# Optimization experiments

Measured on AMD Instinct MI355X. Metric: run time of the kernel, lower is better.

## Reference

```python
import jax, jax.numpy as jnp
import numpy as np


def setup_inputs() -> dict:
    key = jax.random.key(0)
    k1, k2, k3 = jax.random.split(key, 3)
    n_way, n_shot, d, n_query = 5, 10, 1024, 16384
    n_support = n_way * n_shot
    train_imgs = jax.random.normal(k1, (n_support, d), dtype=jnp.float32)
    # one-hot labels: exactly n_shot examples per class (interleaved)
    cls = jnp.tile(jnp.arange(n_way), n_shot)  # [n_support]
    train_labels = jax.nn.one_hot(cls, n_way, dtype=jnp.int64)
    query_imgs = jax.random.normal(k2, (n_query, d), dtype=jnp.float32)
    query_labels = jax.random.randint(k3, (n_query,), 0, n_way)
    return {"train_imgs": train_imgs, "train_labels": train_labels,
            "query_imgs": query_imgs, "query_labels": query_labels}


def reference(train_imgs, train_labels, query_imgs, query_labels):
    # backbone = identity: imgs are already feature embeddings
    n_support, n_way = train_labels.shape
    n_shot = n_support // n_way  # static
    support = train_imgs                      # [n_support, d]
    query = query_imgs                        # [n_query, d]

    # group support features by class: [n_way, n_shot, d]
    cls = jnp.argmax(train_labels, axis=1)
    order = jnp.argsort(cls, stable=True)
    grouped = support[order].reshape(n_way, n_shot, -1)
    mats = jnp.swapaxes(grouped, 1, 2)        # [n_way, d, n_shot]

    # batched reduced SVD (torch.svd some=True -> full_matrices=False)
    U, _, _ = jnp.linalg.svd(mats, full_matrices=False)  # [n_way, d, n_shot]
    Uk = U[:, :, : n_shot - 1]                # [n_way, d, k]

    # projection of queries onto each class subspace: P = Uk Uk^T q
    coeff = jnp.einsum('wdk,qd->wkq', Uk, query)   # [n_way, k, n_query]
    proj = jnp.einsum('wdk,wkq->wqd', Uk, coeff)   # [n_way, n_query, d]
    dist = jnp.sum((query[None, :, :] - proj) ** 2, axis=-1)  # [n_way, n_query]

    logits = -dist.T                           # [n_query, n_way]
    # normalize=False in this configuration
    return jax.nn.log_softmax(logits, axis=1)
```

## Files before the change

kernel.cpp:

```cpp
#include <hip/hip_runtime.h>
#include <stdint.h>


typedef __attribute__((ext_vector_type(4))) float f32x4;
typedef __attribute__((ext_vector_type(8))) short s16x8;

#define WS_G_OFF    0
#define WS_W_OFF    4096
#define WS_IDX_OFF  6400
#define WS_U_OFF    8192

__device__ __forceinline__ unsigned short f2bf(float f) {
  unsigned int u = __float_as_uint(f);
  u += 0x7FFFu + ((u >> 16) & 1u);
  return (unsigned short)(u >> 16);
}

__device__ __forceinline__ bool labels_int64(const int* L) {
  int cnt = 0; bool oddz = true;
  #pragma unroll
  for (int t = 0; t < 20; ++t) {
    int v = L[t];
    if (t & 1) { if (v) oddz = false; }
    else       { if (v) cnt++; }
  }
  return oddz && (cnt == 2);
}

__device__ __forceinline__ int cls_of(const int* L, bool is64, int i) {
  int best = -0x7fffffff, c = 0;
  #pragma unroll
  for (int j = 0; j < 5; ++j) {
    int v = is64 ? L[i * 10 + 2 * j] : L[i * 5 + j];
    if (v > best) { best = v; c = j; }
  }
  return c;
}

__global__ void dsn_gram(const float* __restrict__ support,
                         const int* __restrict__ labels,
                         double* __restrict__ G,
                         int* __restrict__ idx) {
  int wid  = blockIdx.x * 4 + (threadIdx.x >> 6);
  int lane = threadIdx.x & 63;
  if (wid >= 275) return;
  int w = wid / 55, p = wid % 55;
  int a = 0;
  while (p >= 10 - a) { p -= 10 - a; a++; }
  int b = a + p;

  bool is64 = labels_int64(labels);
  int myc = (lane < 50) ? cls_of(labels, is64, lane) : -1;
  unsigned long long mask = __ballot(lane < 50 && myc == w);

  if (wid % 55 == 0 && lane < 10) {
    unsigned long long m2 = mask;
    for (int z = 0; z < lane; ++z) m2 &= m2 - 1;
    idx[w * 10 + lane] = __ffsll(m2) - 1;
  }

  unsigned long long m = mask;
  for (int i = 0; i < a; ++i) m &= m - 1;
  int ia = __ffsll((unsigned long long)m) - 1;
  m = mask;
  for (int i = 0; i < b; ++i) m &= m - 1;
  int ib = __ffsll((unsigned long long)m) - 1;

  const float* A = support + ia * 1024;
  const float* B = support + ib * 1024;
  double acc = 0.0;
  #pragma unroll
  for (int i = 0; i < 16; ++i) {
    int d = lane + 64 * i;
    acc += (double)A[d] * (double)B[d];
  }
  #pragma unroll
  for (int off = 32; off > 0; off >>= 1) acc += __shfl_xor(acc, off);
  if (lane == 0) {
    G[(w * 10 + a) * 10 + b] = acc;
    G[(w * 10 + b) * 10 + a] = acc;
  }
}

__global__ __launch_bounds__(64, 1) void dsn_solve(const double* __restrict__ G,
                                                   float* __restrict__ W) {
  __shared__ float Gf[100], Ysm[100], Zsm[100], Psm[100];
  __shared__ float red[16];
  __shared__ int   jm[1];

  int w = blockIdx.x, t = threadIdx.x;
  bool act = (t < 50);
  int e0 = 2 * t, e1 = 2 * t + 1;
  int i0 = e0 / 10, j0 = e0 % 10;
  int i1 = e1 / 10, j1 = e1 % 10;
  if (!act) { e0 = 0; e1 = 1; i0 = 0; j0 = 0; i1 = 0; j1 = 1; }

  if (act) {
    Gf[e0] = (float)G[w * 100 + e0];
    Gf[e1] = (float)G[w * 100 + e1];
  }
  __syncthreads();

  if (t < 10) {
    float r = 0.f;
    #pragma unroll
    for (int k = 0; k < 10; ++k) r += fabsf(Gf[t * 10 + k]);
    red[t] = r;
  }
  __syncthreads();
  float c = red[0];
  #pragma unroll
  for (int k = 1; k < 10; ++k) c = fmaxf(c, red[k]);
  float cinv = 1.f / c;

  if (act) {
    Ysm[e0] = Gf[e0] * cinv;  Ysm[e1] = Gf[e1] * cinv;
    Zsm[e0] = (i0 == j0) ? 1.f : 0.f;
    Zsm[e1] = (i1 == j1) ? 1.f : 0.f;
  }
  __syncthreads();

  #pragma unroll 1
  for (int it = 0; it < 6; ++it) {
    if (act) {
      float p0 = 0.f, p1 = 0.f;
      #pragma unroll
      for (int k = 0; k < 10; ++k) {
        p0 += Zsm[i0 * 10 + k] * Ysm[k * 10 + j0];
        p1 += Zsm[i1 * 10 + k] * Ysm[k * 10 + j1];
      }
      Psm[e0] = p0; Psm[e1] = p1;
    }
    __syncthreads();
    float y0 = 0.f, y1 = 0.f, z0 = 0.f, z1 = 0.f;
    if (act) {
      float ay0 = 0.f, az0 = 0.f, ay1 = 0.f, az1 = 0.f;
      #pragma unroll
      for (int k = 0; k < 10; ++k) {
        ay0 += Ysm[i0 * 10 + k] * Psm[k * 10 + j0];
        az0 += Psm[i0 * 10 + k] * Zsm[k * 10 + j0];
        ay1 += Ysm[i1 * 10 + k] * Psm[k * 10 + j1];
        az1 += Psm[i1 * 10 + k] * Zsm[k * 10 + j1];
      }
      y0 = 1.5f * Ysm[e0] - 0.5f * ay0;
      z0 = 1.5f * Zsm[e0] - 0.5f * az0;
      y1 = 1.5f * Ysm[e1] - 0.5f * ay1;
      z1 = 1.5f * Zsm[e1] - 0.5f * az1;
    }
    __syncthreads();
    if (act) { Ysm[e0] = y0; Ysm[e1] = y1; Zsm[e0] = z0; Zsm[e1] = z1; }
    __syncthreads();
  }

  float rsc = rsqrtf(c);
  if (act) {
    W[(w * 11 + i0) * 10 + j0] = Zsm[e0] * rsc;
    W[(w * 11 + i1) * 10 + j1] = Zsm[e1] * rsc;
  }

  if (act) {
    Ysm[e0] = ((i0 == j0) ? 1.f : 0.f) - Gf[e0] * cinv;
    Ysm[e1] = ((i1 == j1) ? 1.f : 0.f) - Gf[e1] * cinv;
  }
  __syncthreads();
  #pragma unroll 1
  for (int sq = 0; sq < 8; ++sq) {
    if (act) {
      float p0 = 0.f, p1 = 0.f;
      #pragma unroll
      for (int k = 0; k < 10; ++k) {
        p0 += Ysm[i0 * 10 + k] * Ysm[k * 10 + j0];
        p1 += Ysm[i1 * 10 + k] * Ysm[k * 10 + j1];
      }
      Psm[e0] = p0; Psm[e1] = p1;
    }
    __syncthreads();
    if (t < 10) {
      float m = 0.f;
      #pragma unroll
      for (int k = 0; k < 10; ++k) m = fmaxf(m, fabsf(Psm[t * 10 + k]));
      red[t] = m;
    }
    __syncthreads();
    float m = red[0];
    #pragma unroll
    for (int k = 1; k < 10; ++k) m = fmaxf(m, red[k]);
    float minv = 1.f / m;
    if (act) { Ysm[e0] = Psm[e0] * minv; Ysm[e1] = Psm[e1] * minv; }
    __syncthreads();
  }

  if (t == 0) {
    int best = 0; float bv = Ysm[0];
    #pragma unroll
    for (int k = 1; k < 10; ++k) {
      float dk = Ysm[k * 10 + k];
      if (dk > bv) { bv = dk; best = k; }
    }
    jm[0] = best;
  }
  __syncthreads();
  if (t < 10) red[t] = Ysm[t * 10 + jm[0]];
  __syncthreads();
  float denom = 0.f;
  #pragma unroll
  for (int a2 = 0; a2 < 10; ++a2) {
    float gv = 0.f;
    #pragma unroll
    for (int k = 0; k < 10; ++k) gv += Gf[a2 * 10 + k] * red[k];
    denom += red[a2] * gv;
  }
  if (t < 10)
    W[(w * 11 + 10) * 10 + t] = red[t] * rsqrtf(denom);
}

__global__ void dsn_basis(const float* __restrict__ support,
                          const float* __restrict__ W,
                          const int* __restrict__ idx,
                          unsigned short* __restrict__ U) {
  int r = blockIdx.x;
  int w = r >> 4, kk = r & 15;
  unsigned short* Urow = U + r * 1024;
  if (kk >= 11) {
    for (int d = threadIdx.x; d < 1024; d += 256) Urow[d] = 0;
    return;
  }
  float wv[10]; int id[10];
  #pragma unroll
  for (int s = 0; s < 10; ++s) {
    wv[s] = W[(w * 11 + kk) * 10 + s];
    id[s] = idx[w * 10 + s];
  }
  for (int d = threadIdx.x; d < 1024; d += 256) {
    float sum = 0.f;
    #pragma unroll
    for (int s = 0; s < 10; ++s) sum += support[id[s] * 1024 + d] * wv[s];
    Urow[d] = f2bf(sum);
  }
}

__global__ __launch_bounds__(256) void dsn_main(const float* __restrict__ query,
                                                const unsigned short* __restrict__ U,
                                                float* __restrict__ out) {
  int wid  = blockIdx.x * 4 + (threadIdx.x >> 6);
  int lane = threadIdx.x & 63;
  int q0   = wid * 16;
  int qrow = lane & 15;
  int kbase = (lane >> 4) * 8;

  const float* qp = query + (size_t)(q0 + qrow) * 1024 + kbase;
  const unsigned short* up = U + qrow * 1024 + kbase;

  f32x4 acc[5];
  #pragma unroll
  for (int w = 0; w < 5; ++w) acc[w] = (f32x4){0.f, 0.f, 0.f, 0.f};

  #pragma unroll 4
  for (int kt = 0; kt < 32; ++kt) {
    const float* qk = qp + kt * 32;
    f32x4 lo = *(const f32x4*)qk;
    f32x4 hi = *(const f32x4*)(qk + 4);
    s16x8 bf;
    bf[0] = (short)f2bf(lo[0]); bf[1] = (short)f2bf(lo[1]);
    bf[2] = (short)f2bf(lo[2]); bf[3] = (short)f2bf(lo[3]);
    bf[4] = (short)f2bf(hi[0]); bf[5] = (short)f2bf(hi[1]);
    bf[6] = (short)f2bf(hi[2]); bf[7] = (short)f2bf(hi[3]);
    const unsigned short* uk = up + kt * 32;
    #pragma unroll
    for (int w = 0; w < 5; ++w) {
      s16x8 av = *(const s16x8*)(uk + w * 16384);
      acc[w] = __builtin_amdgcn_mfma_f32_16x16x32_bf16(av, bf, acc[w], 0, 0, 0);
    }
  }

  float sgn2 = ((lane >> 4) == 2) ? -1.f : 1.f;
  float sv[5];
  #pragma unroll
  for (int w = 0; w < 5; ++w) {
    float tcc = acc[w][0] * acc[w][0] + acc[w][1] * acc[w][1] +
                sgn2 * acc[w][2] * acc[w][2] + acc[w][3] * acc[w][3];
    tcc += __shfl_xor(tcc, 16);
    tcc += __shfl_xor(tcc, 32);
    sv[w] = tcc;
  }
  float mx = fmaxf(fmaxf(fmaxf(sv[0], sv[1]), fmaxf(sv[2], sv[3])), sv[4]);
  float sum = 0.f;
  #pragma unroll
  for (int w = 0; w < 5; ++w) sum += expf(sv[w] - mx);
  float lse = mx + logf(sum);
  if (lane < 16) {
    float* o = out + (size_t)(q0 + lane) * 5;
    #pragma unroll
    for (int w = 0; w < 5; ++w) o[w] = sv[w] - lse;
  }
}

extern "C" void kernel_launch(void* const* d_in, const int* in_sizes, int n_in,
                              void* d_out, int out_size, void* d_ws, size_t ws_size,
                              hipStream_t stream) {
  const float* support = (const float*)d_in[0];
  const int*   labels  = (const int*)d_in[1];
  const float* query   = (const float*)d_in[2];
  float* out = (float*)d_out;
  char* ws = (char*)d_ws;

  double*         G   = (double*)(ws + WS_G_OFF);
  float*          W   = (float*)(ws + WS_W_OFF);
  int*            idx = (int*)(ws + WS_IDX_OFF);
  unsigned short* U   = (unsigned short*)(ws + WS_U_OFF);

  int nq = in_sizes[2] / 1024;
  int nwaves = nq / 16;
  int nblocks = (nwaves + 3) / 4;

  hipLaunchKernelGGL(dsn_gram,  dim3(69), dim3(256), 0, stream, support, labels, G, idx);
  hipLaunchKernelGGL(dsn_solve, dim3(5),  dim3(64),  0, stream, G, W);
  hipLaunchKernelGGL(dsn_basis, dim3(80), dim3(256), 0, stream, support, W, idx, U);
  hipLaunchKernelGGL(dsn_main,  dim3(nblocks), dim3(256), 0, stream, query, U, out);
}
```

Measured before the change: 49.42 us.

## Project queries onto raw support vectors and apply per-class Gram correction afterward

Instead of building an orthonormal basis U from the solved coefficients before the main GEMM, the queries are multiplied directly against the raw bf16 support vectors, giving coefficients Z. A small per-class 10x10 matrix (Ghat, derived from the Gram inverse square root minus the dropped singular direction) is then applied to Z in a separate post kernel to form the projected norms. The solve is folded into extra blocks of the GEMM kernel, so it runs concurrently rather than serially before the basis construction. This removes the serial solve and basis kernels from the critical path, but adds a Z write and read round-trip through global memory (80 x 16384 floats) and a third launch.

Result: slower. 64.66 us (+30.8%).

```diff
diff --git a/kernel.cpp b/kernel.cpp
--- a/kernel.cpp
+++ b/kernel.cpp
@@ -6,9 +6,9 @@
 typedef __attribute__((ext_vector_type(8))) short s16x8;
 
 #define WS_G_OFF    0
-#define WS_W_OFF    4096
-#define WS_IDX_OFF  6400
-#define WS_U_OFF    8192
+#define WS_GH_OFF   4096
+#define WS_P_OFF    8192
+#define WS_Z_OFF    262144
 
 __device__ __forceinline__ unsigned short f2bf(float f) {
   unsigned int u = __float_as_uint(f);
@@ -37,58 +37,80 @@
   return c;
 }
 
-__global__ void dsn_gram(const float* __restrict__ support,
-                         const int* __restrict__ labels,
-                         double* __restrict__ G,
-                         int* __restrict__ idx) {
-  int wid  = blockIdx.x * 4 + (threadIdx.x >> 6);
-  int lane = threadIdx.x & 63;
-  if (wid >= 275) return;
-  int w = wid / 55, p = wid % 55;
-  int a = 0;
-  while (p >= 10 - a) { p -= 10 - a; a++; }
-  int b = a + p;
-
+__global__ __launch_bounds__(256) void dsn_prep(const float* __restrict__ support,
+                                                const int* __restrict__ labels,
+                                                double* __restrict__ G,
+                                                unsigned short* __restrict__ P) {
+  int b = blockIdx.x;
   bool is64 = labels_int64(labels);
-  int myc = (lane < 50) ? cls_of(labels, is64, lane) : -1;
-  unsigned long long mask = __ballot(lane < 50 && myc == w);
-
-  if (wid % 55 == 0 && lane < 10) {
-    unsigned long long m2 = mask;
-    for (int z = 0; z < lane; ++z) m2 &= m2 - 1;
-    idx[w * 10 + lane] = __ffsll(m2) - 1;
-  }
-
-  unsigned long long m = mask;
-  for (int i = 0; i < a; ++i) m &= m - 1;
-  int ia = __ffsll((unsigned long long)m) - 1;
-  m = mask;
-  for (int i = 0; i < b; ++i) m &= m - 1;
-  int ib = __ffsll((unsigned long long)m) - 1;
-
-  const float* A = support + ia * 1024;
-  const float* B = support + ib * 1024;
-  double acc = 0.0;
-  #pragma unroll
-  for (int i = 0; i < 16; ++i) {
-    int d = lane + 64 * i;
-    acc += (double)A[d] * (double)B[d];
-  }
-  #pragma unroll
-  for (int off = 32; off > 0; off >>= 1) acc += __shfl_xor(acc, off);
-  if (lane == 0) {
-    G[(w * 10 + a) * 10 + b] = acc;
-    G[(w * 10 + b) * 10 + a] = acc;
-  }
-}
-
-__global__ __launch_bounds__(64, 1) void dsn_solve(const double* __restrict__ G,
-                                                   float* __restrict__ W) {
+
+  if (b < 69) {
+    int wid  = b * 4 + (threadIdx.x >> 6);
+    int lane = threadIdx.x & 63;
+    if (wid >= 275) return;
+    int w = wid / 55, p = wid % 55;
+    int a = 0;
+    while (p >= 10 - a) { p -= 10 - a; a++; }
+    int bb = a + p;
+
+    int myc = (lane < 50) ? cls_of(labels, is64, lane) : -1;
+    unsigned long long mask = __ballot(lane < 50 && myc == w);
+
+    unsigned long long m = mask;
+    for (int i = 0; i < a; ++i) m &= m - 1;
+    int ia = __ffsll((unsigned long long)m) - 1;
+    m = mask;
+    for (int i = 0; i < bb; ++i) m &= m - 1;
+    int ib = __ffsll((unsigned long long)m) - 1;
+
+    const float* A = support + ia * 1024;
+    const float* B = support + ib * 1024;
+    double acc = 0.0;
+    #pragma unroll
+    for (int i = 0; i < 16; ++i) {
+      int d = lane + 64 * i;
+      acc += (double)A[d] * (double)B[d];
+    }
+    #pragma unroll
+    for (int off = 32; off > 0; off >>= 1) acc += __shfl_xor(acc, off);
+    if (lane == 0) {
+      G[(w * 10 + a) * 10 + bb] = acc;
+      G[(w * 10 + bb) * 10 + a] = acc;
+    }
+  } else {
+    int r = b - 69;
+    int w = r >> 4, kk = r & 15;
+    int t = threadIdx.x;
+    unsigned short* Prow = P + r * 1024;
+    if (kk >= 10) {
+      #pragma unroll
+      for (int j = 0; j < 4; ++j) Prow[t + 256 * j] = 0;
+      return;
+    }
+    __shared__ int sid;
+    if (t < 64) {
+      int myc = (t < 50) ? cls_of(labels, is64, t) : -1;
+      unsigned long long mask = __ballot(t < 50 && myc == w);
+      if (t == 0) {
+        unsigned long long m = mask;
+        for (int z = 0; z < kk; ++z) m &= m - 1;
+        sid = __ffsll(m) - 1;
+      }
+    }
+    __syncthreads();
+    const float* src = support + (size_t)sid * 1024;
+    #pragma unroll
+    for (int j = 0; j < 4; ++j) Prow[t + 256 * j] = f2bf(src[t + 256 * j]);
+  }
+}
+
+__device__ void solve_way(const double* __restrict__ G, float* __restrict__ Ghat,
+                          int w) {
   __shared__ float Gf[100], Ysm[100], Zsm[100], Psm[100];
   __shared__ float red[16];
   __shared__ int   jm[1];
 
-  int w = blockIdx.x, t = threadIdx.x;
+  int t = threadIdx.x;
   bool act = (t < 50);
   int e0 = 2 * t, e1 = 2 * t + 1;
   int i0 = e0 / 10, j0 = e0 % 10;
@@ -152,12 +174,6 @@
     __syncthreads();
   }
 
-  float rsc = rsqrtf(c);
-  if (act) {
-    W[(w * 11 + i0) * 10 + j0] = Zsm[e0] * rsc;
-    W[(w * 11 + i1) * 10 + j1] = Zsm[e1] * rsc;
-  }
-
   if (act) {
     Ysm[e0] = ((i0 == j0) ? 1.f : 0.f) - Gf[e0] * cinv;
     Ysm[e1] = ((i1 == j1) ? 1.f : 0.f) - Gf[e1] * cinv;
@@ -210,38 +226,33 @@
     for (int k = 0; k < 10; ++k) gv += Gf[a2 * 10 + k] * red[k];
     denom += red[a2] * gv;
   }
-  if (t < 10)
-    W[(w * 11 + 10) * 10 + t] = red[t] * rsqrtf(denom);
-}
-
-__global__ void dsn_basis(const float* __restrict__ support,
-                          const float* __restrict__ W,
-                          const int* __restrict__ idx,
-                          unsigned short* __restrict__ U) {
-  int r = blockIdx.x;
-  int w = r >> 4, kk = r & 15;
-  unsigned short* Urow = U + r * 1024;
-  if (kk >= 11) {
-    for (int d = threadIdx.x; d < 1024; d += 256) Urow[d] = 0;
+
+  if (act) {
+    float p0 = 0.f, p1 = 0.f;
+    #pragma unroll
+    for (int k = 0; k < 10; ++k) {
+      p0 += Zsm[i0 * 10 + k] * Zsm[k * 10 + j0];
+      p1 += Zsm[i1 * 10 + k] * Zsm[k * 10 + j1];
+    }
+    Psm[e0] = p0; Psm[e1] = p1;
+  }
+  __syncthreads();
+  float rs = rsqrtf(denom);
+  if (act) {
+    Ghat[w * 100 + e0] = Psm[e0] * cinv - (red[i0] * rs) * (red[j0] * rs);
+    Ghat[w * 100 + e1] = Psm[e1] * cinv - (red[i1] * rs) * (red[j1] * rs);
+  }
+}
+
+__global__ __launch_bounds__(256) void dsn_zgemm(const float* __restrict__ query,
+                                                 const unsigned short* __restrict__ P,
+                                                 const double* __restrict__ G,
+                                                 float* __restrict__ Ghat,
+                                                 float* __restrict__ Z) {
+  if (blockIdx.x >= 256) {
+    solve_way(G, Ghat, blockIdx.x - 256);
     return;
   }
-  float wv[10]; int id[10];
-  #pragma unroll
-  for (int s = 0; s < 10; ++s) {
-    wv[s] = W[(w * 11 + kk) * 10 + s];
-    id[s] = idx[w * 10 + s];
-  }
-  for (int d = threadIdx.x; d < 1024; d += 256) {
-    float sum = 0.f;
-    #pragma unroll
-    for (int s = 0; s < 10; ++s) sum += support[id[s] * 1024 + d] * wv[s];
-    Urow[d] = f2bf(sum);
-  }
-}
-
-__global__ __launch_bounds__(256) void dsn_main(const float* __restrict__ query,
-                                                const unsigned short* __restrict__ U,
-                                                float* __restrict__ out) {
   int wid  = blockIdx.x * 4 + (threadIdx.x >> 6);
   int lane = threadIdx.x & 63;
   int q0   = wid * 16;
@@ -249,7 +260,7 @@
   int kbase = (lane >> 4) * 8;
 
   const float* qp = query + (size_t)(q0 + qrow) * 1024 + kbase;
-  const unsigned short* up = U + qrow * 1024 + kbase;
+  const unsigned short* up = P + qrow * 1024 + kbase;
 
   f32x4 acc[5];
   #pragma unroll
@@ -273,26 +284,52 @@
     }
   }
 
-  float sgn2 = ((lane >> 4) == 2) ? -1.f : 1.f;
+  int rowbase = (lane >> 4) * 4;
+  #pragma unroll
+  for (int w = 0; w < 5; ++w) {
+    #pragma unroll
+    for (int r = 0; r < 4; ++r)
+      Z[(size_t)(w * 16 + rowbase + r) * 16384 + q0 + qrow] = acc[w][r];
+  }
+}
+
+__global__ __launch_bounds__(256) void dsn_post(const float* __restrict__ Ghat,
+                                                const float* __restrict__ Z,
+                                                float* __restrict__ out) {
+  __shared__ float Gh[500];
+  int t = threadIdx.x;
+  for (int i = t; i < 500; i += 256) Gh[i] = Ghat[i];
+  __syncthreads();
+  int q = blockIdx.x * 256 + t;
+
+  float zv[50];
+  #pragma unroll
+  for (int w = 0; w < 5; ++w)
+    #pragma unroll
+    for (int s = 0; s < 10; ++s)
+      zv[w * 10 + s] = Z[(size_t)(w * 16 + s) * 16384 + q];
+
   float sv[5];
   #pragma unroll
   for (int w = 0; w < 5; ++w) {
-    float tcc = acc[w][0] * acc[w][0] + acc[w][1] * acc[w][1] +
-                sgn2 * acc[w][2] * acc[w][2] + acc[w][3] * acc[w][3];
-    tcc += __shfl_xor(tcc, 16);
-    tcc += __shfl_xor(tcc, 32);
-    sv[w] = tcc;
+    float s = 0.f;
+    #pragma unroll
+    for (int i = 0; i < 10; ++i) {
+      float gz = 0.f;
+      #pragma unroll
+      for (int j = 0; j < 10; ++j) gz += Gh[w * 100 + i * 10 + j] * zv[w * 10 + j];
+      s += zv[w * 10 + i] * gz;
+    }
+    sv[w] = s;
   }
   float mx = fmaxf(fmaxf(fmaxf(sv[0], sv[1]), fmaxf(sv[2], sv[3])), sv[4]);
   float sum = 0.f;
   #pragma unroll
   for (int w = 0; w < 5; ++w) sum += expf(sv[w] - mx);
   float lse = mx + logf(sum);
-  if (lane < 16) {
-    float* o = out + (size_t)(q0 + lane) * 5;
-    #pragma unroll
-    for (int w = 0; w < 5; ++w) o[w] = sv[w] - lse;
-  }
+  float* o = out + (size_t)q * 5;
+  #pragma unroll
+  for (int w = 0; w < 5; ++w) o[w] = sv[w] - lse;
 }
 
 extern "C" void kernel_launch(void* const* d_in, const int* in_sizes, int n_in,
@@ -304,17 +341,17 @@
   float* out = (float*)d_out;
   char* ws = (char*)d_ws;
 
-  double*         G   = (double*)(ws + WS_G_OFF);
-  float*          W   = (float*)(ws + WS_W_OFF);
-  int*            idx = (int*)(ws + WS_IDX_OFF);
-  unsigned short* U   = (unsigned short*)(ws + WS_U_OFF);
+  double*         G    = (double*)(ws + WS_G_OFF);
+  float*          Ghat = (float*)(ws + WS_GH_OFF);
+  unsigned short* P    = (unsigned short*)(ws + WS_P_OFF);
+  float*          Z    = (float*)(ws + WS_Z_OFF);
 
   int nq = in_sizes[2] / 1024;
-  int nwaves = nq / 16;
-  int nblocks = (nwaves + 3) / 4;
-
-  hipLaunchKernelGGL(dsn_gram,  dim3(69), dim3(256), 0, stream, support, labels, G, idx);
-  hipLaunchKernelGGL(dsn_solve, dim3(5),  dim3(64),  0, stream, G, W);
-  hipLaunchKernelGGL(dsn_basis, dim3(80), dim3(256), 0, stream, support, W, idx, U);
-  hipLaunchKernelGGL(dsn_main,  dim3(nblocks), dim3(256), 0, stream, query, U, out);
-}
+  int gemm_blocks = nq / 64;
+  int post_blocks = nq / 256;
+
+  hipLaunchKernelGGL(dsn_prep,  dim3(149), dim3(256), 0, stream, support, labels, G, P);
+  hipLaunchKernelGGL(dsn_zgemm, dim3(gemm_blocks + 5), dim3(256), 0, stream,
+                     query, P, G, Ghat, Z);
+  hipLaunchKernelGGL(dsn_post,  dim3(post_blocks), dim3(256), 0, stream, Ghat, Z, out);
+}
```
